# Kernel tuning notes

Hardware: AMD Instinct MI355X
Metric: run time of the kernel (lower is better)

## Reference

```python
import jax, jax.numpy as jnp
import numpy as np

G = 60   # rotation group size
K = 13   # SO3 neighbors per group element


def data_process(x, nei):
    # x: [B, C, 60] -> gather neighbors -> [B, C, 60, 13]
    b, c = x.shape[0], x.shape[1]
    return x[:, :, nei].reshape(b, c, G, K)


def comb_conv(x4, W, b):
    # x4: [B, C, 60, 13], W: [O, C, 13] (Conv2d kernel (1,13) squeezed) -> [B, O, 60]
    return jnp.einsum('bcgk,ock->bog', x4, W) + b[None, :, None]


def bn_relu(x, gamma, beta):
    # eval-mode BatchNorm2d folded to per-channel affine, then ReLU
    return jax.nn.relu(x * gamma[None, :, None] + beta[None, :, None])


def group_feat_net(feats, nei, W_in, b_in, W1, b1, g1, be1, W2, b2, g2, be2, Wo, bo, go, beo):
    # Conv_in: plain conv, no BN/ReLU
    d = comb_conv(data_process(feats, nei), W_in, b_in)              # [B,256,60]
    # Residual_Comb_Conv(256,512,256)
    fc = bn_relu(comb_conv(data_process(d, nei), W1, b1), g1, be1)   # [B,512,60]
    fc = bn_relu(comb_conv(data_process(fc, nei), W2, b2), g2, be2)  # [B,256,60]
    d = d + fc
    # Conv_out = Comb_Conv(256,32)
    d = bn_relu(comb_conv(data_process(d, nei), Wo, bo), go, beo)    # [B,32,60]
    eqv = d + feats
    inv = jnp.mean(eqv, axis=-1)                                     # [B,32]
    eqv = eqv / jnp.maximum(jnp.linalg.norm(eqv, axis=1, keepdims=True), 1e-4)
    inv = inv / jnp.maximum(jnp.linalg.norm(inv, axis=1, keepdims=True), 1e-4)
    return inv, eqv


def des2dr(des1, des2, permu):
    # des1, des2: [B,32,60]; permu: [3600] -> gather -> [B,32,60,60]
    b, f = des1.shape[0], des1.shape[1]
    d1p = des1[:, :, permu].reshape(b, f, G, G)
    cor = jnp.einsum('bfag,bfg->ba', d1p, des2)                      # [B,60]
    return jnp.argmax(cor, axis=1)


def setup_inputs() -> dict:
    key = jax.random.key(0)
    ks = jax.random.split(key, 16)
    B = 256
    inp = {
        'feats0': jax.random.normal(ks[0], (B, 32, G), dtype=jnp.float32),
        'feats1': jax.random.normal(ks[1], (B, 32, G), dtype=jnp.float32),
        'true_idx': jax.random.randint(ks[2], (B,), 0, G, dtype=jnp.int32),
        'nei_idx': jax.random.randint(ks[3], (G * K,), 0, G, dtype=jnp.int32),
        'permu_idx': jax.random.randint(ks[4], (G * G,), 0, G, dtype=jnp.int32),
        'W_in': jax.random.normal(ks[5], (256, 32, K), dtype=jnp.float32) * 0.05,
        'b_in': jnp.zeros((256,), dtype=jnp.float32),
        'W1': jax.random.normal(ks[6], (512, 256, K), dtype=jnp.float32) * 0.02,
        'b1': jnp.zeros((512,), dtype=jnp.float32),
        'g1': jnp.ones((512,), dtype=jnp.float32),
        'be1': jnp.zeros((512,), dtype=jnp.float32),
        'W2': jax.random.normal(ks[7], (256, 512, K), dtype=jnp.float32) * 0.02,
        'b2': jnp.zeros((256,), dtype=jnp.float32),
        'g2': jnp.ones((256,), dtype=jnp.float32),
        'be2': jnp.zeros((256,), dtype=jnp.float32),
        'Wo': jax.random.normal(ks[8], (32, 256, K), dtype=jnp.float32) * 0.02,
        'bo': jnp.zeros((32,), dtype=jnp.float32),
        'go': jnp.ones((32,), dtype=jnp.float32),
        'beo': jnp.zeros((32,), dtype=jnp.float32),
    }
    return inp


def reference(feats0, feats1, true_idx, nei_idx, permu_idx,
              W_in, b_in, W1, b1, g1, be1, W2, b2, g2, be2, Wo, bo, go, beo):
    params = (W_in, b_in, W1, b1, g1, be1, W2, b2, g2, be2, Wo, bo, go, beo)
    inv0, eqv0 = group_feat_net(feats0, nei_idx, *params)
    inv1, eqv1 = group_feat_net(feats1, nei_idx, *params)
    pre_idxs = des2dr(eqv0, eqv1, permu_idx)
    ability = jnp.mean((pre_idxs == true_idx).astype(jnp.float32))
    return (feats0, feats1, eqv0, eqv1, inv0, inv1, ability, true_idx, pre_idxs)
```

## Files before the change

### kernel.cpp

```cpp
#include <hip/hip_runtime.h>

#define G60 60
#define KN 13

typedef unsigned int u32;
typedef unsigned short u16;
typedef short short8 __attribute__((ext_vector_type(8)));
typedef float f32x4 __attribute__((ext_vector_type(4)));
typedef float f32x16 __attribute__((ext_vector_type(16)));
typedef u32 u32x4 __attribute__((ext_vector_type(4)));

template <int I> struct Ic { static constexpr int v = I; };
template <int I, int N, typename F>
__device__ __forceinline__ void sfor(F&& f) {
    if constexpr (I < N) { f(Ic<I>{}); sfor<I + 1, N>(f); }
}

__device__ __forceinline__ u32 f32_to_packed(float v) {
    u32 u = __float_as_uint(v);
    u32 hi = (u + 0x7FFFu + ((u >> 16) & 1u)) >> 16;
    float vhi = __uint_as_float(hi << 16);
    float lof = v - vhi;
    u32 ul = __float_as_uint(lof);
    u32 lo = (ul + 0x7FFFu + ((ul >> 16) & 1u)) >> 16;
    return (hi << 16) | lo;
}
__device__ __forceinline__ float packed_f32(u32 w) {
    return __uint_as_float(w & 0xFFFF0000u) + __uint_as_float(w << 16);
}

__device__ __forceinline__ void pack_one(const float* __restrict__ W,
                                         u16* __restrict__ Whi, u16* __restrict__ Wlo,
                                         int C, int O, int CT, int id) {
    int j = id & 7;
    int lane = (id >> 3) & 63;
    int fid = id >> 9;
    int NTt = O >> 5;
    int nt = fid % NTt;
    int t = fid / NTt;
    int SUBS = CT >> 4;
    int sub = t % SUBS;
    int kk = (t / SUBS) % KN;
    int ct = t / (KN * SUBS);
    int q = lane >> 5, n = lane & 31;
    int o = nt * 32 + n;
    int c = ct * CT + sub * 16 + q * 8 + j;
    u32 pw = f32_to_packed(W[((size_t)o * C + c) * KN + kk]);
    Whi[id] = (u16)(pw >> 16);
    Wlo[id] = (u16)(pw & 0xFFFFu);
}

__global__ void __launch_bounds__(256) pack_all_kern(
    const float* W_in, u16* Whi_in, u16* Wlo_in,
    const float* W1, u16* Whi_1, u16* Wlo_1,
    const float* W2, u16* Whi_2, u16* Wlo_2,
    const float* Wo, u16* Whi_o, u16* Wlo_o) {
    const int T0 = KN * 32 * 256;
    const int T1 = T0 + KN * 256 * 512;
    const int T2 = T1 + KN * 512 * 256;
    const int T3 = T2 + KN * 256 * 32;
    int id = blockIdx.x * 256 + threadIdx.x;
    if (id < T0) pack_one(W_in, Whi_in, Wlo_in, 32, 256, 32, id);
    else if (id < T1) pack_one(W1, Whi_1, Wlo_1, 256, 512, 64, id - T0);
    else if (id < T2) pack_one(W2, Whi_2, Wlo_2, 512, 256, 64, id - T1);
    else if (id < T3) pack_one(Wo, Whi_o, Wlo_o, 256, 32, 64, id - T2);
}

template <int CT, int WM, int WN, int SRC, bool BNR, bool OUTF32>
__global__ void __launch_bounds__(256, 2) mconv11(
    const u32* __restrict__ Xp, const float* __restrict__ Xf0,
    const float* __restrict__ Xf1,
    const float* __restrict__ pIn,
    const float* __restrict__ bnb, const float* __restrict__ bng,
    const float* __restrict__ bnB,
    const u32* __restrict__ resid,
    const u16* __restrict__ Whi, const u16* __restrict__ Wlo,
    const float* __restrict__ bias, const float* __restrict__ gamma,
    const float* __restrict__ beta,
    const int* __restrict__ nei,
    u32* __restrict__ outp, float* __restrict__ outf,
    int C, int O, int tpz, int bbase, int NBb) {
    constexpr int SUBS = CT >> 4;
    constexpr int S = KN * SUBS;
    constexpr int NG = S / 2;
    constexpr int STRIDE = CT + 8;
    constexpr int PLSZ = G60 * STRIDE;
    constexpr int NMG = 4 / WM;
    constexpr int NRO = (WM == 4) ? 2 : WM;
    __shared__ u16 Xs[4 * PLSZ];
    const int tid = threadIdx.x;
    const int lane = tid & 63;
    const int wv = tid >> 6;
    const int mg = wv % NMG;
    const int ng = wv / NMG;
    const int q = lane >> 5;
    const int m = lane & 31;
    const int bp = (int)blockIdx.x + (bbase >> 1);
    const int NTt = O >> 5;
    const int nt0 = (int)blockIdx.y * (WM * WN) + ng * WN;
    const int ct0 = (int)blockIdx.z * tpz;
    const size_t PLi = (size_t)NBb * C * G60;
    float* outfz = OUTF32 ? (outf + (size_t)blockIdx.z * ((size_t)NBb * O * G60)) : nullptr;

    int rowoff[NRO][KN];
#pragma unroll
    for (int jj = 0; jj < NRO; ++jj) {
        int mts, base;
        if (WM == 4) { mts = jj; base = 0; }
        else {
            int s = mg * WM + jj;
            mts = s & 1;
            base = (s >> 1) * 2 * PLSZ;
        }
        int g = mts * 32 + m;
        int gl = (g < G60) ? g : 0;
#pragma unroll
        for (int kk = 0; kk < KN; ++kk)
            rowoff[jj][kk] = nei[gl * KN + kk] * STRIDE + base;
    }

    f32x16 acc[WM][WN];
#pragma unroll
    for (int j = 0; j < WM; ++j)
#pragma unroll
        for (int nt = 0; nt < WN; ++nt) acc[j][nt] = (f32x16)(0.f);

    short8 Bh[2][2][WN], Bl[2][2][WN];

    for (int ct = ct0; ct < ct0 + tpz; ++ct) {
        const size_t fbase = ((size_t)(ct * S) * NTt + nt0) * 512 + (size_t)lane * 8;

        __syncthreads();
        constexpr int PAIRS = (CT / 2) * G60;
        for (int i = tid; i < 2 * PAIRS; i += 256) {
            int sb = (i >= PAIRS) ? 1 : 0;
            int r = i - sb * PAIRS;
            int ccp = (r * 17477) >> 20;
            int g = r - ccp * G60;
            int cc = ccp * 2;
            const int bg = bp * 2 + sb;
            const int bloc = bg - bbase;
            u32 w0, w1;
            if (SRC == 0) {
                size_t cg0 = ((size_t)bloc * C + (size_t)ct * CT + cc) * G60 + g;
                w0 = Xp[cg0]; w1 = Xp[cg0 + G60];
            } else if (SRC == 1) {
                const float* Xf = (bg >= 256) ? Xf1 : Xf0;
                size_t cg0 = ((size_t)(bg & 255) * C + (size_t)ct * CT + cc) * G60 + g;
                w0 = f32_to_packed(Xf[cg0]); w1 = f32_to_packed(Xf[cg0 + G60]);
            } else {
                size_t cg0 = ((size_t)bloc * C + (size_t)ct * CT + cc) * G60 + g;
                int c0 = ct * CT + cc;
                float v0 = pIn[cg0] + pIn[PLi + cg0];
                float v1 = pIn[cg0 + G60] + pIn[PLi + cg0 + G60];
                v0 = fmaxf((v0 + bnb[c0]) * bng[c0] + bnB[c0], 0.f) + packed_f32(resid[cg0]);
                v1 = fmaxf((v1 + bnb[c0 + 1]) * bng[c0 + 1] + bnB[c0 + 1], 0.f) + packed_f32(resid[cg0 + G60]);
                w0 = f32_to_packed(v0); w1 = f32_to_packed(v1);
            }
            int rb = sb * 2 * PLSZ + g * STRIDE + cc;
            *(u32*)(Xs + rb) = (w0 >> 16) | (w1 & 0xFFFF0000u);
            *(u32*)(Xs + rb + PLSZ) = (w0 & 0xFFFFu) | (w1 << 16);
        }

        sfor<0, 2>([&](auto uc) {
            constexpr int u = decltype(uc)::v;
            sfor<0, WN>([&](auto nc) {
                constexpr int nt = decltype(nc)::v;
                const size_t fb = fbase + ((size_t)u * NTt + nt) * 512;
                Bh[0][u][nt] = *reinterpret_cast<const short8*>(Whi + fb);
                Bl[0][u][nt] = *reinterpret_cast<const short8*>(Wlo + fb);
            });
        });
        __syncthreads();

        sfor<0, NG>([&](auto gc) {
            constexpr int g = decltype(gc)::v;
            constexpr int pb = g & 1;
            if constexpr (g + 1 < NG) {
                constexpr int pn = (g + 1) & 1;
                sfor<0, 2>([&](auto uc) {
                    constexpr int u = decltype(uc)::v;
                    constexpr int s = 2 * (g + 1) + u;
                    sfor<0, WN>([&](auto nc) {
                        constexpr int nt = decltype(nc)::v;
                        const size_t fb = fbase + ((size_t)s * NTt + nt) * 512;
                        Bh[pn][u][nt] = *reinterpret_cast<const short8*>(Whi + fb);
                        Bl[pn][u][nt] = *reinterpret_cast<const short8*>(Wlo + fb);
                    });
                });
            }
            short8 Ah[2][WM], Al[2][WM];
            sfor<0, 2>([&](auto uc) {
                constexpr int u = decltype(uc)::v;
                constexpr int s = 2 * g + u;
                constexpr int kk = s / SUBS;
                constexpr int sub = s - kk * SUBS;
                sfor<0, WM>([&](auto jc) {
                    constexpr int j = decltype(jc)::v;
                    int off;
                    if constexpr (WM == 4)
                        off = rowoff[j & 1][kk] + (j >> 1) * 2 * PLSZ + sub * 16 + q * 8;
                    else
                        off = rowoff[j][kk] + sub * 16 + q * 8;
                    Ah[u][j] = *reinterpret_cast<const short8*>(Xs + off);
                    Al[u][j] = *reinterpret_cast<const short8*>(Xs + off + PLSZ);
                });
            });
            sfor<0, 2>([&](auto uc) {
                constexpr int u = decltype(uc)::v;
                sfor<0, WN>([&](auto nc) {
                    constexpr int nt = decltype(nc)::v;
                    sfor<0, WM>([&](auto jc) {
                        constexpr int j = decltype(jc)::v;
                        acc[j][nt] = __builtin_amdgcn_mfma_f32_32x32x16_bf16(
                            Ah[u][j], Bh[pb][u][nt], acc[j][nt], 0, 0, 0);
                    });
                });
                sfor<0, WN>([&](auto nc) {
                    constexpr int nt = decltype(nc)::v;
                    sfor<0, WM>([&](auto jc) {
                        constexpr int j = decltype(jc)::v;
                        acc[j][nt] = __builtin_amdgcn_mfma_f32_32x32x16_bf16(
                            Ah[u][j], Bl[pb][u][nt], acc[j][nt], 0, 0, 0);
                    });
                });
                sfor<0, WN>([&](auto nc) {
                    constexpr int nt = decltype(nc)::v;
                    sfor<0, WM>([&](auto jc) {
                        constexpr int j = decltype(jc)::v;
                        acc[j][nt] = __builtin_amdgcn_mfma_f32_32x32x16_bf16(
                            Al[u][j], Bh[pb][u][nt], acc[j][nt], 0, 0, 0);
                    });
                });
            });
        });
    }

#pragma unroll
    for (int j = 0; j < WM; ++j) {
        const int s = mg * WM + j;
        const int bbs = s >> 1, mts = s & 1;
        const int bloc = bp * 2 + bbs - bbase;
#pragma unroll
        for (int nt = 0; nt < WN; ++nt) {
            const int o = (nt0 + nt) * 32 + m;
            float bi = 0.f, ga = 1.f, be = 0.f;
            if (!OUTF32) { bi = bias[o]; if (BNR) { ga = gamma[o]; be = beta[o]; } }
#pragma unroll
            for (int grp = 0; grp < 4; ++grp) {
                const int g0 = mts * 32 + grp * 8 + q * 4;
                if (g0 < G60) {
                    size_t oi = ((size_t)bloc * O + o) * G60 + g0;
                    if (OUTF32) {
                        f32x4 v;
#pragma unroll
                        for (int rr = 0; rr < 4; ++rr) v[rr] = acc[j][nt][grp * 4 + rr];
                        *reinterpret_cast<f32x4*>(outfz + oi) = v;
                    } else {
                        u32x4 pv;
#pragma unroll
                        for (int rr = 0; rr < 4; ++rr) {
                            float v = acc[j][nt][grp * 4 + rr] + bi;
                            if (BNR) v = fmaxf(v * ga + be, 0.f);
                            pv[rr] = f32_to_packed(v);
                        }
                        *reinterpret_cast<u32x4*>(outp + oi) = pv;
                    }
                }
            }
        }
    }
}

__global__ void __launch_bounds__(64) finalize_kern(
    const float* __restrict__ pout,
    const float* __restrict__ feats0, const float* __restrict__ feats1,
    const float* __restrict__ bo, const float* __restrict__ go,
    const float* __restrict__ beo,
    float* __restrict__ of0, float* __restrict__ of1,
    float* __restrict__ oe0, float* __restrict__ oe1,
    float* __restrict__ oi0, float* __restrict__ oi1,
    int bbase, int NBb) {
    const int bloc = blockIdx.x;
    const int bg = bloc + bbase;
    const int net = bg >> 8;
    const int bl = bg & 255;
    const float* feats = net ? feats1 : feats0;
    float* out_feats = net ? of1 : of0;
    float* out_eqv = net ? oe1 : oe0;
    float* out_inv = net ? oi1 : oi0;
    const size_t PB = (size_t)NBb * 32 * G60;
    __shared__ float E[32 * G60];
    __shared__ float gnorm[G60];
    __shared__ float inv_pre[32];
    __shared__ float inv_nrm;
    const int tid = threadIdx.x;

    for (int i = tid; i < 32 * G60; i += 64) {
        int f = i / G60;
        size_t idx = (size_t)bloc * 1920 + i;
        size_t idf = (size_t)bl * 1920 + i;
        float ft = feats[idf];
        out_feats[idf] = ft;
        float s = pout[idx] + pout[PB + idx] + pout[2 * PB + idx] + pout[3 * PB + idx];
        float v = fmaxf((s + bo[f]) * go[f] + beo[f], 0.f);
        E[i] = v + ft;
    }
    __syncthreads();
    if (tid < G60) {
        float s = 0.f;
        for (int f = 0; f < 32; ++f) { float v = E[f * G60 + tid]; s += v * v; }
        gnorm[tid] = fmaxf(sqrtf(s), 1e-4f);
    }
    if (tid < 32) {
        float s = 0.f;
        for (int g = 0; g < G60; ++g) s += E[tid * G60 + g];
        inv_pre[tid] = s / 60.f;
    }
    __syncthreads();
    if (tid == 0) {
        float s = 0.f;
        for (int f = 0; f < 32; ++f) s += inv_pre[f] * inv_pre[f];
        inv_nrm = fmaxf(sqrtf(s), 1e-4f);
    }
    __syncthreads();
    for (int i = tid; i < 1920; i += 64) {
        int g = i % G60;
        out_eqv[(size_t)bl * 1920 + i] = E[i] / gnorm[g];
    }
    if (tid < 32) out_inv[bl * 32 + tid] = inv_pre[tid] / inv_nrm;
}

__global__ void __launch_bounds__(256) des2dr_kern(
    const float* __restrict__ e0f, const float* __restrict__ e1f,
    const int* __restrict__ permu, int* __restrict__ pre_int,
    float* __restrict__ out_pre) {
    const int b = blockIdx.x;
    __shared__ float X0[32 * G60];
    __shared__ float X1[32 * G60];
    __shared__ float pc[256];
    __shared__ float cor[64];
    const int tid = threadIdx.x;
    for (int i = tid; i < 1920; i += 256) {
        X0[i] = e0f[(size_t)b * 1920 + i];
        X1[i] = e1f[(size_t)b * 1920 + i];
    }
    __syncthreads();
    const int a = tid >> 2, fc = tid & 3;
    float s = 0.f;
    if (a < G60) {
        for (int g = 0; g < G60; ++g) {
            int p = permu[a * G60 + g];
#pragma unroll
            for (int f = fc * 8; f < fc * 8 + 8; ++f) s += X0[f * G60 + p] * X1[f * G60 + g];
        }
    }
    pc[tid] = s;
    __syncthreads();
    if (tid < 64) cor[tid] = pc[4 * tid] + pc[4 * tid + 1] + pc[4 * tid + 2] + pc[4 * tid + 3];
    __syncthreads();
    if (tid == 0) {
        float best = cor[0];
        int bi = 0;
        for (int a2 = 1; a2 < G60; ++a2)
            if (cor[a2] > best) { best = cor[a2]; bi = a2; }
        pre_int[b] = bi;
        out_pre[b] = (float)bi;
    }
}

__global__ void __launch_bounds__(256) ability_kern(
    const int* __restrict__ pre_int, const int* __restrict__ true_idx,
    float* __restrict__ out_ability, float* __restrict__ out_true) {
    __shared__ int cnt[256];
    const int t = threadIdx.x;
    cnt[t] = (pre_int[t] == true_idx[t]) ? 1 : 0;
    out_true[t] = (float)true_idx[t];
    __syncthreads();
    for (int s = 128; s > 0; s >>= 1) {
        if (t < s) cnt[t] += cnt[t + s];
        __syncthreads();
    }
    if (t == 0) out_ability[0] = (float)cnt[0] / 256.0f;
}

extern "C" void kernel_launch(void* const* d_in, const int* in_sizes, int n_in,
                              void* d_out, int out_size, void* d_ws, size_t ws_size,
                              hipStream_t stream) {
    const float* feats0 = (const float*)d_in[0];
    const float* feats1 = (const float*)d_in[1];
    const int* true_idx = (const int*)d_in[2];
    const int* nei = (const int*)d_in[3];
    const int* permu = (const int*)d_in[4];
    const float* W_in = (const float*)d_in[5];
    const float* b_in = (const float*)d_in[6];
    const float* W1 = (const float*)d_in[7];
    const float* b1 = (const float*)d_in[8];
    const float* g1 = (const float*)d_in[9];
    const float* be1 = (const float*)d_in[10];
    const float* W2 = (const float*)d_in[11];
    const float* b2 = (const float*)d_in[12];
    const float* g2 = (const float*)d_in[13];
    const float* be2 = (const float*)d_in[14];
    const float* Wo = (const float*)d_in[15];
    const float* bo = (const float*)d_in[16];
    const float* go = (const float*)d_in[17];
    const float* beo = (const float*)d_in[18];

    float* out = (float*)d_out;
    const size_t SZF = (size_t)256 * 32 * G60;
    float* out_f0 = out;
    float* out_f1 = out + SZF;
    float* out_e0 = out + 2 * SZF;
    float* out_e1 = out + 3 * SZF;
    float* out_i0 = out + 4 * SZF;
    float* out_i1 = out_i0 + 256 * 32;
    float* out_ab = out_i1 + 256 * 32;
    float* out_tr = out_ab + 1;
    float* out_pr = out_tr + 256;

    char* p = (char*)d_ws;
    auto alloc = [&](size_t bytes) { char* r = p; p += (bytes + 255) & ~(size_t)255; return r; };
    const size_t NW_IN = (size_t)KN * 32 * 256;
    const size_t NW_1 = (size_t)KN * 256 * 512;
    const size_t NW_2 = (size_t)KN * 512 * 256;
    const size_t NW_O = (size_t)KN * 256 * 32;
    u16* Whi_in = (u16*)alloc(NW_IN * 2); u16* Wlo_in = (u16*)alloc(NW_IN * 2);
    u16* Whi_1 = (u16*)alloc(NW_1 * 2);   u16* Wlo_1 = (u16*)alloc(NW_1 * 2);
    u16* Whi_2 = (u16*)alloc(NW_2 * 2);   u16* Wlo_2 = (u16*)alloc(NW_2 * 2);
    u16* Whi_o = (u16*)alloc(NW_O * 2);   u16* Wlo_o = (u16*)alloc(NW_O * 2);

    const size_t MERGED_NEED = 173000000;
    const bool merged = ws_size >= MERGED_NEED;

    {
        int total = KN * (32 * 256 + 256 * 512 + 512 * 256 + 256 * 32);
        pack_all_kern<<<dim3((total + 255) / 256), dim3(256), 0, stream>>>(
            W_in, Whi_in, Wlo_in, W1, Whi_1, Wlo_1, W2, Whi_2, Wlo_2, Wo, Whi_o, Wlo_o);
    }

    if (merged) {
        u32* dbuf = (u32*)alloc((size_t)512 * 256 * G60 * 4);
        u32* fcbuf = (u32*)alloc((size_t)512 * 512 * G60 * 4);
        float* p2 = (float*)alloc((size_t)2 * 512 * 256 * G60 * 4);
        float* pout = (float*)fcbuf;
        int* pre_int = (int*)alloc(512 * 4);

        mconv11<32, 2, 1, 1, false, false><<<dim3(256, 4, 1), dim3(256), 0, stream>>>(
            nullptr, feats0, feats1, nullptr, nullptr, nullptr, nullptr, nullptr,
            Whi_in, Wlo_in, b_in, nullptr, nullptr, nei, dbuf, nullptr,
            32, 256, 1, 0, 512);
        mconv11<64, 4, 1, 0, true, false><<<dim3(256, 4, 1), dim3(256), 0, stream>>>(
            dbuf, nullptr, nullptr, nullptr, nullptr, nullptr, nullptr, nullptr,
            Whi_1, Wlo_1, b1, g1, be1, nei, fcbuf, nullptr,
            256, 512, 4, 0, 512);
        mconv11<64, 4, 1, 0, false, true><<<dim3(256, 2, 2), dim3(256), 0, stream>>>(
            fcbuf, nullptr, nullptr, nullptr, nullptr, nullptr, nullptr, nullptr,
            Whi_2, Wlo_2, nullptr, nullptr, nullptr, nei, nullptr, p2,
            512, 256, 4, 0, 512);
        mconv11<64, 1, 1, 2, false, true><<<dim3(256, 1, 4), dim3(256), 0, stream>>>(
            nullptr, nullptr, nullptr, p2, b2, g2, be2, dbuf,
            Whi_o, Wlo_o, nullptr, nullptr, nullptr, nei, nullptr, pout,
            256, 32, 1, 0, 512);
        finalize_kern<<<dim3(512), dim3(64), 0, stream>>>(
            pout, feats0, feats1, bo, go, beo,
            out_f0, out_f1, out_e0, out_e1, out_i0, out_i1, 0, 512);
    } else {
        u32* dbuf = (u32*)alloc((size_t)256 * 256 * G60 * 4);
        u32* fcbuf = (u32*)alloc((size_t)256 * 512 * G60 * 4);
        float* p2 = (float*)alloc((size_t)2 * 256 * 256 * G60 * 4);
        float* pout = (float*)alloc((size_t)4 * SZF * 4);
        int* pre_int0 = (int*)alloc(256 * 4);

        for (int net = 0; net < 2; ++net) {
            const int bb = net * 256;
            mconv11<32, 2, 1, 1, false, false><<<dim3(128, 4, 1), dim3(256), 0, stream>>>(
                nullptr, feats0, feats1, nullptr, nullptr, nullptr, nullptr, nullptr,
                Whi_in, Wlo_in, b_in, nullptr, nullptr, nei, dbuf, nullptr,
                32, 256, 1, bb, 256);
            mconv11<64, 4, 1, 0, true, false><<<dim3(128, 4, 1), dim3(256), 0, stream>>>(
                dbuf, nullptr, nullptr, nullptr, nullptr, nullptr, nullptr, nullptr,
                Whi_1, Wlo_1, b1, g1, be1, nei, fcbuf, nullptr,
                256, 512, 4, bb, 256);
            mconv11<64, 4, 1, 0, false, true><<<dim3(128, 2, 2), dim3(256), 0, stream>>>(
                fcbuf, nullptr, nullptr, nullptr, nullptr, nullptr, nullptr, nullptr,
                Whi_2, Wlo_2, nullptr, nullptr, nullptr, nei, nullptr, p2,
                512, 256, 4, bb, 256);
            mconv11<64, 1, 1, 2, false, true><<<dim3(128, 1, 4), dim3(256), 0, stream>>>(
                nullptr, nullptr, nullptr, p2, b2, g2, be2, dbuf,
                Whi_o, Wlo_o, nullptr, nullptr, nullptr, nei, nullptr, pout,
                256, 32, 1, bb, 256);
            finalize_kern<<<dim3(256), dim3(64), 0, stream>>>(
                pout, feats0, feats1, bo, go, beo,
                out_f0, out_f1, out_e0, out_e1, out_i0, out_i1, bb, 256);
        }
        des2dr_kern<<<dim3(256), dim3(256), 0, stream>>>(out_e0, out_e1, permu, pre_int0, out_pr);
        ability_kern<<<dim3(1), dim3(256), 0, stream>>>(pre_int0, true_idx, out_ab, out_tr);
        (void)in_sizes; (void)n_in; (void)out_size;
        return;
    }

    {
        int* pre_int = (int*)alloc(256 * 4);
        des2dr_kern<<<dim3(256), dim3(256), 0, stream>>>(out_e0, out_e1, permu, pre_int, out_pr);
        ability_kern<<<dim3(1), dim3(256), 0, stream>>>(pre_int, true_idx, out_ab, out_tr);
    }

    (void)in_sizes; (void)n_in; (void)out_size; (void)ws_size;
}
```

Baseline: 720.9 us.

## Cut register pressure in comb-conv kernel for higher occupancy

The neighbor row-offset table moves from per-thread registers into shared memory, and the weight double-buffer is replaced by a single-step prefetch of the hi weights only. Launch bounds are raised to 4 blocks per SM. The two middle convs switch their wave tiling from 4x1 to 2x2 so weight fragments are shared across wave rows. The aim is higher occupancy to hide gather and global-load latency, at the cost of extra LDS reads for the offsets and less load/compute overlap within a wave.

After: 742.2 us. 3.0% more time.

```diff
diff --git a/kernel.cpp b/kernel.cpp
--- a/kernel.cpp
+++ b/kernel.cpp
@@ -67,7 +67,7 @@
 }
 
 template <int CT, int WM, int WN, int SRC, bool BNR, bool OUTF32>
-__global__ void __launch_bounds__(256, 2) mconv11(
+__global__ void __launch_bounds__(256, 4) mconv12(
     const u32* __restrict__ Xp, const float* __restrict__ Xf0,
     const float* __restrict__ Xf1,
     const float* __restrict__ pIn,
@@ -82,12 +82,11 @@
     int C, int O, int tpz, int bbase, int NBb) {
     constexpr int SUBS = CT >> 4;
     constexpr int S = KN * SUBS;
-    constexpr int NG = S / 2;
     constexpr int STRIDE = CT + 8;
     constexpr int PLSZ = G60 * STRIDE;
     constexpr int NMG = 4 / WM;
-    constexpr int NRO = (WM == 4) ? 2 : WM;
     __shared__ u16 Xs[4 * PLSZ];
+    __shared__ int rofftab[KN * 64];
     const int tid = threadIdx.x;
     const int lane = tid & 63;
     const int wv = tid >> 6;
@@ -102,21 +101,18 @@
     const size_t PLi = (size_t)NBb * C * G60;
     float* outfz = OUTF32 ? (outf + (size_t)blockIdx.z * ((size_t)NBb * O * G60)) : nullptr;
 
-    int rowoff[NRO][KN];
-#pragma unroll
-    for (int jj = 0; jj < NRO; ++jj) {
-        int mts, base;
-        if (WM == 4) { mts = jj; base = 0; }
-        else {
-            int s = mg * WM + jj;
-            mts = s & 1;
-            base = (s >> 1) * 2 * PLSZ;
-        }
-        int g = mts * 32 + m;
-        int gl = (g < G60) ? g : 0;
-#pragma unroll
-        for (int kk = 0; kk < KN; ++kk)
-            rowoff[jj][kk] = nei[gl * KN + kk] * STRIDE + base;
+    for (int i = tid; i < KN * 64; i += 256) {
+        int kk = i >> 6, gi = i & 63;
+        int gl = (gi < G60) ? gi : 0;
+        rofftab[i] = nei[gl * KN + kk] * STRIDE;
+    }
+
+    int bbc[WM], tidx[WM];
+#pragma unroll
+    for (int j = 0; j < WM; ++j) {
+        int s = mg * WM + j;
+        bbc[j] = (s >> 1) * 2 * PLSZ;
+        tidx[j] = (s & 1) * 32 + m;
     }
 
     f32x16 acc[WM][WN];
@@ -124,8 +120,6 @@
     for (int j = 0; j < WM; ++j)
 #pragma unroll
         for (int nt = 0; nt < WN; ++nt) acc[j][nt] = (f32x16)(0.f);
-
-    short8 Bh[2][2][WN], Bl[2][2][WN];
 
     for (int ct = ct0; ct < ct0 + tpz; ++ct) {
         const size_t fbase = ((size_t)(ct * S) * NTt + nt0) * 512 + (size_t)lane * 8;
@@ -162,77 +156,79 @@
             *(u32*)(Xs + rb + PLSZ) = (w0 & 0xFFFFu) | (w1 << 16);
         }
 
-        sfor<0, 2>([&](auto uc) {
-            constexpr int u = decltype(uc)::v;
+        short8 BhC[WN];
+        sfor<0, WN>([&](auto nc) {
+            constexpr int nt = decltype(nc)::v;
+            BhC[nt] = *reinterpret_cast<const short8*>(Whi + fbase + (size_t)nt * 512);
+        });
+        __syncthreads();
+
+        int roff[WM];
+        sfor<0, S>([&](auto sc) {
+            constexpr int s = decltype(sc)::v;
+            constexpr int kk = s / SUBS;
+            constexpr int sub = s - kk * SUBS;
+            if constexpr (sub == 0) {
+                sfor<0, WM>([&](auto jc) {
+                    constexpr int j = decltype(jc)::v;
+                    roff[j] = rofftab[kk * 64 + tidx[j]];
+                });
+            }
+            short8 Ah[WM], Bl[WN];
+            sfor<0, WM>([&](auto jc) {
+                constexpr int j = decltype(jc)::v;
+                const int off = roff[j] + bbc[j] + sub * 16 + q * 8;
+                Ah[j] = *reinterpret_cast<const short8*>(Xs + off);
+            });
             sfor<0, WN>([&](auto nc) {
                 constexpr int nt = decltype(nc)::v;
-                const size_t fb = fbase + ((size_t)u * NTt + nt) * 512;
-                Bh[0][u][nt] = *reinterpret_cast<const short8*>(Whi + fb);
-                Bl[0][u][nt] = *reinterpret_cast<const short8*>(Wlo + fb);
+                Bl[nt] = *reinterpret_cast<const short8*>(
+                    Wlo + fbase + ((size_t)s * NTt + nt) * 512);
             });
-        });
-        __syncthreads();
-
-        sfor<0, NG>([&](auto gc) {
-            constexpr int g = decltype(gc)::v;
-            constexpr int pb = g & 1;
-            if constexpr (g + 1 < NG) {
-                constexpr int pn = (g + 1) & 1;
-                sfor<0, 2>([&](auto uc) {
-                    constexpr int u = decltype(uc)::v;
-                    constexpr int s = 2 * (g + 1) + u;
-                    sfor<0, WN>([&](auto nc) {
-                        constexpr int nt = decltype(nc)::v;
-                        const size_t fb = fbase + ((size_t)s * NTt + nt) * 512;
-                        Bh[pn][u][nt] = *reinterpret_cast<const short8*>(Whi + fb);
-                        Bl[pn][u][nt] = *reinterpret_cast<const short8*>(Wlo + fb);
-                    });
+            sfor<0, WN>([&](auto nc) {
+                constexpr int nt = decltype(nc)::v;
+                sfor<0, WM>([&](auto jc) {
+                    constexpr int j = decltype(jc)::v;
+                    acc[j][nt] = __builtin_amdgcn_mfma_f32_32x32x16_bf16(
+                        Ah[j], BhC[nt], acc[j][nt], 0, 0, 0);
+                });
+            });
+            sfor<0, WN>([&](auto nc) {
+                constexpr int nt = decltype(nc)::v;
+                sfor<0, WM>([&](auto jc) {
+                    constexpr int j = decltype(jc)::v;
+                    acc[j][nt] = __builtin_amdgcn_mfma_f32_32x32x16_bf16(
+                        Ah[j], Bl[nt], acc[j][nt], 0, 0, 0);
+                });
+            });
+            short8 Al[WM];
+            sfor<0, WM>([&](auto jc) {
+                constexpr int j = decltype(jc)::v;
+                const int off = roff[j] + bbc[j] + sub * 16 + q * 8;
+                Al[j] = *reinterpret_cast<const short8*>(Xs + off + PLSZ);
+            });
+            short8 BhN[WN];
+            if constexpr (s + 1 < S) {
+                sfor<0, WN>([&](auto nc) {
+                    constexpr int nt = decltype(nc)::v;
+                    BhN[nt] = *reinterpret_cast<const short8*>(
+                        Whi + fbase + ((size_t)(s + 1) * NTt + nt) * 512);
                 });
             }
-            short8 Ah[2][WM], Al[2][WM];
-            sfor<0, 2>([&](auto uc) {
-                constexpr int u = decltype(uc)::v;
-                constexpr int s = 2 * g + u;
-                constexpr int kk = s / SUBS;
-                constexpr int sub = s - kk * SUBS;
+            sfor<0, WN>([&](auto nc) {
+                constexpr int nt = decltype(nc)::v;
                 sfor<0, WM>([&](auto jc) {
                     constexpr int j = decltype(jc)::v;
-                    int off;
-                    if constexpr (WM == 4)
-                        off = rowoff[j & 1][kk] + (j >> 1) * 2 * PLSZ + sub * 16 + q * 8;
-                    else
-                        off = rowoff[j][kk] + sub * 16 + q * 8;
-                    Ah[u][j] = *reinterpret_cast<const short8*>(Xs + off);
-                    Al[u][j] = *reinterpret_cast<const short8*>(Xs + off + PLSZ);
+                    acc[j][nt] = __builtin_amdgcn_mfma_f32_32x32x16_bf16(
+                        Al[j], BhC[nt], acc[j][nt], 0, 0, 0);
                 });
             });
-            sfor<0, 2>([&](auto uc) {
-                constexpr int u = decltype(uc)::v;
+            if constexpr (s + 1 < S) {
                 sfor<0, WN>([&](auto nc) {
                     constexpr int nt = decltype(nc)::v;
-                    sfor<0, WM>([&](auto jc) {
-                        constexpr int j = decltype(jc)::v;
-                        acc[j][nt] = __builtin_amdgcn_mfma_f32_32x32x16_bf16(
-                            Ah[u][j], Bh[pb][u][nt], acc[j][nt], 0, 0, 0);
-                    });
+                    BhC[nt] = BhN[nt];
                 });
-                sfor<0, WN>([&](auto nc) {
-                    constexpr int nt = decltype(nc)::v;
-                    sfor<0, WM>([&](auto jc) {
-                        constexpr int j = decltype(jc)::v;
-                        acc[j][nt] = __builtin_amdgcn_mfma_f32_32x32x16_bf16(
-                            Ah[u][j], Bl[pb][u][nt], acc[j][nt], 0, 0, 0);
-                    });
-                });
-                sfor<0, WN>([&](auto nc) {
-                    constexpr int nt = decltype(nc)::v;
-                    sfor<0, WM>([&](auto jc) {
-                        constexpr int j = decltype(jc)::v;
-                        acc[j][nt] = __builtin_amdgcn_mfma_f32_32x32x16_bf16(
-                            Al[u][j], Bh[pb][u][nt], acc[j][nt], 0, 0, 0);
-                    });
-                });
-            });
+            }
         });
     }
 
@@ -446,25 +442,28 @@
         float* pout = (float*)fcbuf;
         int* pre_int = (int*)alloc(512 * 4);
 
-        mconv11<32, 2, 1, 1, false, false><<<dim3(256, 4, 1), dim3(256), 0, stream>>>(
+        mconv12<32, 2, 1, 1, false, false><<<dim3(256, 4, 1), dim3(256), 0, stream>>>(
             nullptr, feats0, feats1, nullptr, nullptr, nullptr, nullptr, nullptr,
             Whi_in, Wlo_in, b_in, nullptr, nullptr, nei, dbuf, nullptr,
             32, 256, 1, 0, 512);
-        mconv11<64, 4, 1, 0, true, false><<<dim3(256, 4, 1), dim3(256), 0, stream>>>(
+        mconv12<64, 2, 2, 0, true, false><<<dim3(256, 4, 1), dim3(256), 0, stream>>>(
             dbuf, nullptr, nullptr, nullptr, nullptr, nullptr, nullptr, nullptr,
             Whi_1, Wlo_1, b1, g1, be1, nei, fcbuf, nullptr,
             256, 512, 4, 0, 512);
-        mconv11<64, 4, 1, 0, false, true><<<dim3(256, 2, 2), dim3(256), 0, stream>>>(
+        mconv12<64, 2, 2, 0, false, true><<<dim3(256, 2, 2), dim3(256), 0, stream>>>(
             fcbuf, nullptr, nullptr, nullptr, nullptr, nullptr, nullptr, nullptr,
             Whi_2, Wlo_2, nullptr, nullptr, nullptr, nei, nullptr, p2,
             512, 256, 4, 0, 512);
-        mconv11<64, 1, 1, 2, false, true><<<dim3(256, 1, 4), dim3(256), 0, stream>>>(
+        mconv12<64, 1, 1, 2, false, true><<<dim3(256, 1, 4), dim3(256), 0, stream>>>(
             nullptr, nullptr, nullptr, p2, b2, g2, be2, dbuf,
             Whi_o, Wlo_o, nullptr, nullptr, nullptr, nei, nullptr, pout,
             256, 32, 1, 0, 512);
         finalize_kern<<<dim3(512), dim3(64), 0, stream>>>(
             pout, feats0, feats1, bo, go, beo,
             out_f0, out_f1, out_e0, out_e1, out_i0, out_i1, 0, 512);
+
+        des2dr_kern<<<dim3(256), dim3(256), 0, stream>>>(out_e0, out_e1, permu, pre_int, out_pr);
+        ability_kern<<<dim3(1), dim3(256), 0, stream>>>(pre_int, true_idx, out_ab, out_tr);
     } else {
         u32* dbuf = (u32*)alloc((size_t)256 * 256 * G60 * 4);
         u32* fcbuf = (u32*)alloc((size_t)256 * 512 * G60 * 4);
@@ -474,19 +473,19 @@
 
         for (int net = 0; net < 2; ++net) {
             const int bb = net * 256;
-            mconv11<32, 2, 1, 1, false, false><<<dim3(128, 4, 1), dim3(256), 0, stream>>>(
+            mconv12<32, 2, 1, 1, false, false><<<dim3(128, 4, 1), dim3(256), 0, stream>>>(
                 nullptr, feats0, feats1, nullptr, nullptr, nullptr, nullptr, nullptr,
                 Whi_in, Wlo_in, b_in, nullptr, nullptr, nei, dbuf, nullptr,
                 32, 256, 1, bb, 256);
-            mconv11<64, 4, 1, 0, true, false><<<dim3(128, 4, 1), dim3(256), 0, stream>>>(
+            mconv12<64, 2, 2, 0, true, false><<<dim3(128, 4, 1), dim3(256), 0, stream>>>(
                 dbuf, nullptr, nullptr, nullptr, nullptr, nullptr, nullptr, nullptr,
                 Whi_1, Wlo_1, b1, g1, be1, nei, fcbuf, nullptr,
                 256, 512, 4, bb, 256);
-            mconv11<64, 4, 1, 0, false, true><<<dim3(128, 2, 2), dim3(256), 0, stream>>>(
+            mconv12<64, 2, 2, 0, false, true><<<dim3(128, 2, 2), dim3(256), 0, stream>>>(
                 fcbuf, nullptr, nullptr, nullptr, nullptr, nullptr, nullptr, nullptr,
                 Whi_2, Wlo_2, nullptr, nullptr, nullptr, nei, nullptr, p2,
                 512, 256, 4, bb, 256);
-            mconv11<64, 1, 1, 2, false, true><<<dim3(128, 1, 4), dim3(256), 0, stream>>>(
+            mconv12<64, 1, 1, 2, false, true><<<dim3(128, 1, 4), dim3(256), 0, stream>>>(
                 nullptr, nullptr, nullptr, p2, b2, g2, be2, dbuf,
                 Whi_o, Wlo_o, nullptr, nullptr, nullptr, nei, nullptr, pout,
                 256, 32, 1, bb, 256);
@@ -496,14 +495,6 @@
         }
         des2dr_kern<<<dim3(256), dim3(256), 0, stream>>>(out_e0, out_e1, permu, pre_int0, out_pr);
         ability_kern<<<dim3(1), dim3(256), 0, stream>>>(pre_int0, true_idx, out_ab, out_tr);
-        (void)in_sizes; (void)n_in; (void)out_size;
-        return;
-    }
-
-    {
-        int* pre_int = (int*)alloc(256 * 4);
-        des2dr_kern<<<dim3(256), dim3(256), 0, stream>>>(out_e0, out_e1, permu, pre_int, out_pr);
-        ability_kern<<<dim3(1), dim3(256), 0, stream>>>(pre_int, true_idx, out_ab, out_tr);
     }
 
     (void)in_sizes; (void)n_in; (void)out_size; (void)ws_size;
```
